# Optimization experiments

Measured on AMD Instinct MI355X. Metric: run time of the kernel, lower is better.

The kernel has to match this reference:

```python
import jax, jax.numpy as jnp
import numpy as np

L = 512          # profile HMM model length (number of match states)
S = 25           # alphabet size (input_dim)
BATCH = 128
T_LEN = 1024
TINY = np.finfo(np.float32).tiny


def setup_inputs():
    key = jax.random.key(0)
    ks = jax.random.split(key, 18)
    def n(k, shape):
        return 0.1 * jax.random.normal(k, shape, dtype=jnp.float32)
    return {
        "seq": jax.random.randint(ks[0], (BATCH, T_LEN), 0, S),
        "em_kernel": n(ks[1], (L, S)),
        "ins_kernel": n(ks[2], (S,)),
        "flank_kernel": n(ks[3], (1,)),
        "btm": n(ks[4], (L,)),
        "m2e": n(ks[5], (L,)),
        "mtm": n(ks[6], (L - 1,)),
        "m2i": n(ks[7], (L - 1,)),
        "i2m": n(ks[8], (L - 1,)),
        "i2i": n(ks[9], (L - 1,)),
        "mtd": n(ks[10], (L,)),
        "dtm": n(ks[11], (L,)),
        "dtd": n(ks[12], (L - 1,)),
        "lf_loop": n(ks[13], (1,)),
        "lf_exit": n(ks[14], (1,)),
        "e2u": n(ks[15], (1,)),
        "e2r": n(ks[16], (1,)),
        "e2t": n(ks[17], (1,)),
    }


def _build_hmm(em_kernel, ins_kernel, flank_kernel, btm, m2e, mtm, m2i, i2m, i2i,
               mtd, dtm, dtd, lf_loop, lf_exit, e2u, e2r, e2t):
    """Build implicit transition matrix A [q,q], emission matrix B [q,S+1], init dist [q].
    Explicit states begin/end/delete are marginalized out (silent states), yielding the
    implicit transition structure of the profile HMM (match skips via delete chains)."""
    Lm = em_kernel.shape[0]
    q = 2 * Lm + 3                      # LF, M_1..M_L, I_1..I_{L-1}, U, RF, T
    U, RF, TM = 2 * Lm, 2 * Lm + 1, 2 * Lm + 2
    idx = jnp.arange(Lm)
    dt = em_kernel.dtype
    # per-source-state softmax over explicit outgoing edges
    begin_p = jax.nn.softmax(jnp.concatenate([btm, mtd[:1]]))            # begin -> M_j / D_1
    btm_p = begin_p[:Lm]
    mp = jax.nn.softmax(jnp.stack([mtm, m2i, m2e[:Lm - 1], mtd[1:]], axis=-1), axis=-1)
    mtm_p, m2i_p, m2e_p, mtd_mid = mp[:, 0], mp[:, 1], mp[:, 2], mp[:, 3]
    ip = jax.nn.softmax(jnp.stack([i2m, i2i], axis=-1), axis=-1)
    i2m_p, i2i_p = ip[:, 0], ip[:, 1]
    dp = jax.nn.softmax(jnp.stack([dtm[:Lm - 1], dtd], axis=-1), axis=-1)
    dtm_p = jnp.concatenate([dp[:, 0], jnp.ones((1,), dt)])              # D_L -> end with prob 1
    dtd_p = dp[:, 1]
    fp = jax.nn.softmax(jnp.concatenate([lf_loop, lf_exit]))            # shared flank kernels
    floop, fexit = fp[0], fp[1]
    ep = jax.nn.softmax(jnp.concatenate([e2u, e2r, e2t]))               # end -> U / RF / T
    # marginalize silent delete chain. Sk[i,k]: P(src_i => target via deletes),
    # src_0 = begin, src_i = M_i; target M_{k+2} for k<=L-2, end for k=L-1.
    mtd_p = jnp.concatenate([begin_p[Lm:], mtd_mid])                    # begin->D_1, M_i->D_{i+1}
    cp_log = jnp.concatenate([jnp.zeros((1,), dt), jnp.cumsum(jnp.log(dtd_p))])
    Sk = mtd_p[:, None] * jnp.exp(cp_log[None, :] - cp_log[:, None]) * dtm_p[None, :]
    Sk = jnp.where(idx[None, :] >= idx[:, None], Sk, jnp.zeros((), dt))
    enter = btm_p + jnp.pad(Sk[0, :Lm - 1], (1, 0))                      # begin => M_j
    begin_end = Sk[0, Lm - 1]                                            # begin => end (all deleted)
    m2e_tot = jnp.concatenate([m2e_p + Sk[1:, Lm - 1], jnp.ones((1,), dt)])
    A = jnp.zeros((q, q), dt)
    Mblk = jnp.zeros((Lm, Lm), dt).at[idx[:-1], idx[1:]].set(mtm_p)
    Mblk = Mblk.at[0:Lm - 1, 1:Lm].add(Sk[1:Lm, 0:Lm - 1])               # match skips (j>=i+2)
    A = A.at[1:Lm + 1, 1:Lm + 1].set(Mblk)
    A = A.at[0, 0].set(floop)
    A = A.at[0, 1:Lm + 1].set(fexit * enter)
    A = A.at[0, U].set(fexit * begin_end * ep[0])
    A = A.at[0, RF].set(fexit * begin_end * ep[1])
    A = A.at[0, TM].set(fexit * begin_end * ep[2])
    A = A.at[jnp.arange(1, Lm), jnp.arange(Lm + 1, 2 * Lm)].set(m2i_p)   # M_i -> I_i
    A = A.at[1:Lm + 1, U].set(m2e_tot * ep[0])
    A = A.at[1:Lm + 1, RF].set(m2e_tot * ep[1])
    A = A.at[1:Lm + 1, TM].set(m2e_tot * ep[2])
    A = A.at[jnp.arange(Lm + 1, 2 * Lm), jnp.arange(2, Lm + 1)].set(i2m_p)  # I_i -> M_{i+1}
    A = A.at[jnp.arange(Lm + 1, 2 * Lm), jnp.arange(Lm + 1, 2 * Lm)].set(i2i_p)
    A = A.at[U, 1:Lm + 1].set(fexit * enter)
    A = A.at[U, U].set(floop + fexit * begin_end * ep[0])
    A = A.at[U, RF].set(fexit * begin_end * ep[1])
    A = A.at[U, TM].set(fexit * begin_end * ep[2])
    A = A.at[RF, RF].set(floop)
    A = A.at[RF, TM].set(fexit)
    A = A.at[TM, TM].set(1.0)
    # emission matrix per make_default_emission_matrix: [ins; em; ins x (L+1)] rows,
    # softmax, zero pad column, terminal one-hot row -> [2L+3, S+1]
    rows = jnp.concatenate([ins_kernel[None], em_kernel,
                            jnp.tile(ins_kernel[None], (Lm + 1, 1))], axis=0)
    Bm = jax.nn.softmax(rows, axis=-1)
    Bm = jnp.concatenate([Bm, jnp.zeros((2 * Lm + 2, 1), dt)], axis=-1)
    s_alph = em_kernel.shape[1]
    Bm = jnp.concatenate([Bm, jax.nn.one_hot(jnp.array([s_alph]), s_alph + 1, dtype=dt)], axis=0)
    # initial distribution: start in left flank w.p. sigmoid(flank_init), else enter model
    p0 = jax.nn.sigmoid(flank_kernel[0])
    init = jnp.zeros((q,), dt).at[0].set(p0)
    init = init.at[1:Lm + 1].set((1 - p0) * enter)
    init = init.at[U].set((1 - p0) * begin_end * ep[0])
    init = init.at[RF].set((1 - p0) * begin_end * ep[1])
    init = init.at[TM].set((1 - p0) * begin_end * ep[2])
    return A, Bm, init


def _forward(seq, *params):
    A, Bm, init = _build_hmm(*params)
    # emission probs per timestep: matvec(B, one_hot(x)) == column gather
    E = Bm.T[seq]                        # [batch, T, q]
    alpha = init[None, :] * E[:, 0]
    s = alpha.sum(-1, keepdims=True) + TINY
    ll = jnp.log(s[:, 0])
    alpha = alpha / s

    def step(carry, Et):
        a, l = carry
        a = Et * (a @ A)                 # forward-algorithm recurrence + scaling
        sn = a.sum(-1, keepdims=True) + TINY
        return (a / sn, l + jnp.log(sn[:, 0])), None

    (alpha, ll), _ = jax.lax.scan(step, (alpha, ll), jnp.swapaxes(E[:, 1:], 0, 1))
    return ll                            # [batch] sequence log-likelihoods


def reference(seq, em_kernel, ins_kernel, flank_kernel, btm, m2e, mtm, m2i, i2m, i2i,
              mtd, dtm, dtd, lf_loop, lf_exit, e2u, e2r, e2t):
    return _forward(seq, em_kernel, ins_kernel, flank_kernel, btm, m2e, mtm, m2i, i2m,
                    i2i, mtd, dtm, dtd, lf_loop, lf_exit, e2u, e2r, e2t)
```

## Files before the change

### kernel.cpp

```cpp
#include <hip/hip_runtime.h>
#include <math.h>

#define LM 512
#define TLEN 1024
#define TINY_F 1.17549435e-38f

#define OFF_ENTER 0
#define OFF_MTM   512
#define OFF_I2M   1024
#define OFF_DTM   1536
#define OFF_WC    2048
#define OFF_MC    2560
#define OFF_M2I   3072
#define OFF_I2I   3584
#define OFF_M2E   4096
#define OFF_INS   4608
#define OFF_SC    4640
#define OFF_EMB   5120

typedef float v2f __attribute__((ext_vector_type(2)));

__device__ __forceinline__ v2f pfma(v2f a, v2f b, v2f c) {
    return __builtin_elementwise_fma(a, b, c);
}
__device__ __forceinline__ v2f vs(float c) { return (v2f){c, c}; }

template<int Ctrl, int RowMask>
__device__ __forceinline__ float fdpp(float oldv, float src) {
    int r = __builtin_amdgcn_update_dpp(
        __builtin_bit_cast(int, oldv), __builtin_bit_cast(int, src),
        Ctrl, RowMask, 0xF, false);
    return __builtin_bit_cast(float, r);
}

template<int Ctrl, int RowMask>
__device__ __forceinline__ float fdppb(float src) {
    int r = __builtin_amdgcn_update_dpp(
        0, __builtin_bit_cast(int, src),
        Ctrl, RowMask, 0xF, true);
    return __builtin_bit_cast(float, r);
}

__device__ __forceinline__ float rdlane63(float v) {
    return __builtin_bit_cast(float,
        __builtin_amdgcn_readlane(__builtin_bit_cast(int, v), 63));
}

__device__ __forceinline__ float wave_sum_to63(float v) {
    v += fdpp<0x111, 0xF>(0.f, v);
    v += fdpp<0x112, 0xF>(0.f, v);
    v += fdpp<0x114, 0xF>(0.f, v);
    v += fdpp<0x118, 0xF>(0.f, v);
    v += fdpp<0x142, 0xA>(0.f, v);
    v += fdpp<0x143, 0xC>(0.f, v);
    return v;
}

__global__ __launch_bounds__(512) void hmm_setup(
    const float* __restrict__ ins,
    const float* __restrict__ flank, const float* __restrict__ btm,
    const float* __restrict__ m2e, const float* __restrict__ mtm,
    const float* __restrict__ m2i, const float* __restrict__ i2m,
    const float* __restrict__ i2i, const float* __restrict__ mtd,
    const float* __restrict__ dtm, const float* __restrict__ dtd,
    const float* __restrict__ lfl, const float* __restrict__ lfe,
    const float* __restrict__ e2u, const float* __restrict__ e2r,
    const float* __restrict__ e2t, float* __restrict__ P)
{
    __shared__ float beginp[513];
    __shared__ float mtdp[512], dtmp[512], dtdp[512], cplog[512];
    __shared__ float mtmp[512], m2ip[512], m2ep[512], i2mp[512], i2ip[512];
    __shared__ float rbuf[512], rbuf2[512];
    const int j = threadIdx.x;

    if (j < 25) {
        float sm = 0.f;
        for (int s = 0; s < 25; ++s) sm += expf(ins[s]);
        P[OFF_INS + j] = log2f(expf(ins[j]) / sm);
    }

    float eb = expf(btm[j]);
    rbuf[j] = eb;
    __syncthreads();
    for (int s = 256; s > 0; s >>= 1) {
        if (j < s) rbuf[j] += rbuf[j + s];
        __syncthreads();
    }
    float e512 = expf(mtd[0]);
    float tot = rbuf[0] + e512;
    beginp[j] = eb / tot;
    if (j == 0) { beginp[512] = e512 / tot; mtdp[0] = e512 / tot; }

    if (j < 511) {
        float a = expf(mtm[j]), b = expf(m2i[j]), c = expf(m2e[j]), d = expf(mtd[j + 1]);
        float s = a + b + c + d;
        mtmp[j] = a / s; m2ip[j] = b / s; m2ep[j] = c / s; mtdp[j + 1] = d / s;
        float ia = expf(i2m[j]), ib = expf(i2i[j]); s = ia + ib;
        i2mp[j] = ia / s; i2ip[j] = ib / s;
        float da = expf(dtm[j]), db = expf(dtd[j]); s = da + db;
        dtmp[j] = da / s; dtdp[j] = db / s;
    }
    if (j == 511) dtmp[511] = 1.0f;
    __syncthreads();

    {
        float lw = (j >= 1) ? logf(dtdp[j - 1]) : 0.f;
        rbuf[j] = lw;
        __syncthreads();
        float* bufs[2] = { rbuf, rbuf2 };
        int cur = 0;
        for (int off = 1; off < 512; off <<= 1) {
            float v = bufs[cur][j];
            if (j >= off) v += bufs[cur][j - off];
            bufs[cur ^ 1][j] = v;
            cur ^= 1;
            __syncthreads();
        }
        cplog[j] = bufs[cur][j];
    }
    __syncthreads();

    if (j == 0) {
        float fl = expf(lfl[0]), fe = expf(lfe[0]); float fs = fl + fe;
        float floop = fl / fs, fexit = fe / fs;
        float eu = expf(e2u[0]), er = expf(e2r[0]), et = expf(e2t[0]);
        float es = eu + er + et; float ep0 = eu / es, ep1 = er / es;
        float p0 = 1.0f / (1.0f + expf(-flank[0]));
        P[OFF_SC + 0] = floop;
        P[OFF_SC + 1] = fexit;
        P[OFF_SC + 2] = p0;
        P[OFF_SC + 5] = ep0;
        P[OFF_SC + 6] = ep1;
        P[OFF_SC + 9] = 1.0f - p0;
    }
    __syncthreads();

    float en = beginp[j];
    if (j >= 1) en += mtdp[0] * expf(cplog[j - 1]) * dtmp[j - 1];
    P[OFF_ENTER + j] = en;
    P[OFF_MTM + j] = (j >= 1) ? mtmp[j - 1] : 0.f;
    P[OFF_I2M + j] = (j >= 1) ? i2mp[j - 1] : 0.f;
    P[OFF_DTM + j] = (j >= 1) ? dtmp[j - 1] : 0.f;
    P[OFF_WC  + j] = (j >= 1) ? mtdp[j]     : 0.f;
    P[OFF_MC  + j] = (j >= 1) ? dtdp[j - 1] : 0.f;
    P[OFF_M2I + j] = (j < 511) ? m2ip[j] : 0.f;
    P[OFF_I2I + j] = (j < 511) ? i2ip[j] : 0.f;
    P[OFF_M2E + j] = (j < 511)
        ? (m2ep[j] + mtdp[j + 1] * expf(cplog[511] - cplog[j + 1]))
        : 1.0f;
}

__global__ __launch_bounds__(64) void hmm_emrel(
    const float* __restrict__ em, const float* __restrict__ ins,
    float* __restrict__ P)
{
    const int j = blockIdx.x * 64 + threadIdx.x;

    float sm = 0.f;
    for (int s = 0; s < 25; ++s) sm += expf(ins[s]);

    const float* row = em + j * 25;
    float mx = row[0];
    for (int s = 1; s < 25; ++s) mx = fmaxf(mx, row[s]);
    float sme = 0.f;
    for (int s = 0; s < 25; ++s) sme += expf(row[s] - mx);
    float inv = 1.0f / sme;

    int lanej = j >> 3, e = j & 7;
    int pos = ((e >> 2) << 8) | (lanej << 2) | (e & 3);
    for (int s = 0; s < 25; ++s) {
        float inspS = expf(ins[s]) / sm;
        P[OFF_EMB + s * 512 + pos] = (expf(row[s] - mx) * inv) / inspS;
    }
}

__global__ __launch_bounds__(64, 1) void hmm_forward(
    const int* __restrict__ seq, const float* __restrict__ P,
    float* __restrict__ out)
{
    __shared__ float sLogEi[32];
    __shared__ __align__(16) int sSeq[TLEN + 4];

    const int lane = threadIdx.x;
    const int b = blockIdx.x;
    const int base = lane * 8;
    const float* __restrict__ EmG = P + OFF_EMB;

    {
        if (lane < 32) sLogEi[lane] = P[OFF_INS + (lane < 25 ? lane : 0)];
        const int4* s4 = (const int4*)(seq + b * TLEN);
        int4* d4 = (int4*)sSeq;
#pragma unroll
        for (int k = lane; k < 256; k += 64) d4[k] = s4[k];
        if (lane < 4) sSeq[TLEN + lane] = 0;
    }
    __syncthreads();

    float llE;
    {
        float le = 0.f;
#pragma unroll
        for (int k = 0; k < 16; ++k) le += sLogEi[sSeq[lane * 16 + k]];
        llE = rdlane63(wave_sum_to63(le));
    }

    float mtm_[8], dtm_[8], wC_[8], mC_[8];
    v2f enter2[4], enterF2[4], m2iS2[4], i2i2[4], m2e2[4], dtmM2[4], invNX2[4];
    {
        float enter_[8], m2iS_[8], i2i_[8], m2e_[8], dtmM_[8], invNX_[8];
#pragma unroll
        for (int e = 0; e < 8; ++e) {
            enter_[e] = P[OFF_ENTER + base + e];
            mtm_[e]   = P[OFF_MTM + base + e];
            dtm_[e]   = P[OFF_DTM + base + e];
            wC_[e]    = P[OFF_WC + base + e];
            mC_[e]    = P[OFF_MC + base + e];
            i2i_[e]   = P[OFF_I2I + base + e];
            m2e_[e]   = P[OFF_M2E + base + e];
            float i2mN = (base + e + 1 < 512) ? P[OFF_I2M + base + e + 1] : 1.0f;
            m2iS_[e]  = P[OFF_M2I + base + e] * i2mN;
            invNX_[e] = 1.0f / i2mN;
        }
        float Mp = mC_[0];
        dtmM_[0] = dtm_[0];
#pragma unroll
        for (int e = 1; e < 8; ++e) { dtmM_[e] = dtm_[e] * Mp; Mp *= mC_[e]; }
#pragma unroll
        for (int p = 0; p < 4; ++p) {
            enter2[p] = (v2f){enter_[2*p], enter_[2*p+1]};
            m2iS2[p]  = (v2f){m2iS_[2*p],  m2iS_[2*p+1]};
            i2i2[p]   = (v2f){i2i_[2*p],   i2i_[2*p+1]};
            m2e2[p]   = (v2f){m2e_[2*p],   m2e_[2*p+1]};
            dtmM2[p]  = (v2f){dtmM_[2*p],  dtmM_[2*p+1]};
            invNX2[p] = (v2f){invNX_[2*p], invNX_[2*p+1]};
        }
    }
    const float floop = P[OFF_SC + 0], fexit = P[OFF_SC + 1], p0 = P[OFF_SC + 2];
    const float ep0 = P[OFF_SC + 5], ep1 = P[OFF_SC + 6];
    const float omp0 = P[OFF_SC + 9];
    const v2f floop2 = vs(floop);
    const v2f epv2 = (v2f){ep0, ep1};
#pragma unroll
    for (int p = 0; p < 4; ++p) enterF2[p] = enter2[p] * vs(fexit);

    v2f am2[4], ci2[4];
#define AM(e) ((e) & 1 ? am2[(e) >> 1].y : am2[(e) >> 1].x)
#define CI(e) ((e) & 1 ? ci2[(e) >> 1].y : ci2[(e) >> 1].x)

    v2f EmA2[4], EmB2[4];
    {
        int s0 = sSeq[0];
        const float4* c4 = (const float4*)(EmG + (s0 << 9) + (lane << 2));
        float4 xx = c4[0], yy = c4[64];
        EmA2[0] = (v2f){xx.x, xx.y}; EmA2[1] = (v2f){xx.z, xx.w};
        EmA2[2] = (v2f){yy.x, yy.y}; EmA2[3] = (v2f){yy.z, yy.w};
    }
#pragma unroll
    for (int p = 0; p < 4; ++p) {
        am2[p] = EmA2[p] * vs(omp0) * enter2[p];
        ci2[p] = (v2f){0.f, 0.f};
    }
    v2f GR = (v2f){p0, 0.f};
    float ll2 = llE;

    int symN = sSeq[1];
    {
        const float4* c4 = (const float4*)(EmG + (symN << 9) + (lane << 2));
        float4 xx = c4[0], yy = c4[64];
        EmA2[0] = (v2f){xx.x, xx.y}; EmA2[1] = (v2f){xx.z, xx.w};
        EmA2[2] = (v2f){yy.x, yy.y}; EmA2[3] = (v2f){yy.z, yy.w};
    }
    symN = sSeq[2];
    int sidx = 3;

#define STEP(EmC2, EmN2, DO_NORM)                                              \
  {                                                                            \
    {    \
      const float4* c4 = (const float4*)(EmG + (symN << 9) + (lane << 2));     \
      float4 xx = c4[0], yy = c4[64];                                          \
      EmN2[0] = (v2f){xx.x, xx.y}; EmN2[1] = (v2f){xx.z, xx.w};                \
      EmN2[2] = (v2f){yy.x, yy.y}; EmN2[3] = (v2f){yy.z, yy.w};                \
      symN = sSeq[sidx]; ++sidx;                                               \
    }                                                                          \
    float amL = fdppb<0x138, 0xF>(am2[3].y);                                   \
    float ciL = fdppb<0x138, 0xF>(ci2[3].y);                                   \
                 \
    float Apre[8];                                                             \
    Apre[0] = amL * wC_[0];                                                    \
    _Pragma("unroll")                                                          \
    for (int e = 1; e < 8; ++e)                                                \
      Apre[e] = fmaf(Apre[e - 1], mC_[e], AM(e - 1) * wC_[e]);                 \
         \
    float carry = fdppb<0x138, 0xF>(Apre[7]);                                  \
                \
    v2f dv = am2[0] * m2e2[0];                                                 \
    dv = pfma(am2[1], m2e2[1], dv);                                            \
    dv = pfma(am2[2], m2e2[2], dv);                                            \
    dv = pfma(am2[3], m2e2[3], dv);                                            \
    float dsum = rdlane63(wave_sum_to63(dv.x + dv.y));                         \
              \
    float Gold = GR.x;                                                         \
    GR = pfma(vs(dsum), epv2, GR * floop2);                                    \
       \
    v2f tp[4];                                                                 \
    tp[0].x = fmaf(amL, mtm_[0], ciL);                                         \
    tp[0].y = fmaf(AM(0), mtm_[1], CI(0));                                     \
    tp[1].x = fmaf(AM(1), mtm_[2], CI(1));                                     \
    tp[1].y = fmaf(AM(2), mtm_[3], CI(2));                                     \
    tp[2].x = fmaf(AM(3), mtm_[4], CI(3));                                     \
    tp[2].y = fmaf(AM(4), mtm_[5], CI(4));                                     \
    tp[3].x = fmaf(AM(5), mtm_[6], CI(5));                                     \
    tp[3].y = fmaf(AM(6), mtm_[7], CI(6));                                     \
                       \
    ci2[0] = pfma(am2[0], m2iS2[0], ci2[0] * i2i2[0]);                         \
    ci2[1] = pfma(am2[1], m2iS2[1], ci2[1] * i2i2[1]);                         \
    ci2[2] = pfma(am2[2], m2iS2[2], ci2[2] * i2i2[2]);                         \
    ci2[3] = pfma(am2[3], m2iS2[3], ci2[3] * i2i2[3]);                         \
          \
    v2f Gold2 = vs(Gold), carry2 = vs(carry);                                  \
    tp[0] = pfma(Gold2, enterF2[0], tp[0]);                                    \
    tp[1] = pfma(Gold2, enterF2[1], tp[1]);                                    \
    tp[2] = pfma(Gold2, enterF2[2], tp[2]);                                    \
    tp[3] = pfma(Gold2, enterF2[3], tp[3]);                                    \
    tp[0].y = fmaf(dtm_[1], Apre[0], tp[0].y);                                 \
    tp[1].x = fmaf(dtm_[2], Apre[1], tp[1].x);                                 \
    tp[1].y = fmaf(dtm_[3], Apre[2], tp[1].y);                                 \
    tp[2].x = fmaf(dtm_[4], Apre[3], tp[2].x);                                 \
    tp[2].y = fmaf(dtm_[5], Apre[4], tp[2].y);                                 \
    tp[3].x = fmaf(dtm_[6], Apre[5], tp[3].x);                                 \
    tp[3].y = fmaf(dtm_[7], Apre[6], tp[3].y);                                 \
    tp[0] = pfma(dtmM2[0], carry2, tp[0]);                                     \
    tp[1] = pfma(dtmM2[1], carry2, tp[1]);                                     \
    tp[2] = pfma(dtmM2[2], carry2, tp[2]);                                     \
    tp[3] = pfma(dtmM2[3], carry2, tp[3]);                                     \
    am2[0] = EmC2[0] * tp[0];                                                  \
    am2[1] = EmC2[1] * tp[1];                                                  \
    am2[2] = EmC2[2] * tp[2];                                                  \
    am2[3] = EmC2[3] * tp[3];                                                  \
      \
                                      \
    if (DO_NORM) {                                                             \
      v2f ns = pfma(ci2[0], invNX2[0], am2[0]);                                \
      ns += pfma(ci2[1], invNX2[1], am2[1]);                                   \
      ns += pfma(ci2[2], invNX2[2], am2[2]);                                   \
      ns += pfma(ci2[3], invNX2[3], am2[3]);                                   \
      float sl = ns.x + ns.y + ((lane == 0) ? (GR.x + GR.y) : 0.f);            \
      float s = rdlane63(wave_sum_to63(sl)) + TINY_F;                          \
      ll2 += __log2f(s);                                                       \
      float inv = 1.0f / s;                                                    \
      v2f inv2 = vs(inv);                                                      \
      am2[0] *= inv2; am2[1] *= inv2; am2[2] *= inv2; am2[3] *= inv2;          \
      ci2[0] *= inv2; ci2[1] *= inv2; ci2[2] *= inv2; ci2[3] *= inv2;          \
      GR *= inv2;                                                              \
    }                                                                          \
  }

#define PAIR(NORM2)                                                            \
    STEP(EmA2, EmB2, 0)                                                        \
    STEP(EmB2, EmA2, NORM2)

    for (int c = 0; c < 63; ++c) {
        int nf = ((c & 3) == 3);
        PAIR(0) PAIR(0) PAIR(0) PAIR(0)
        PAIR(0) PAIR(0) PAIR(0) PAIR(nf)
    }
    for (int p = 0; p < 7; ++p) {
        PAIR(0)
    }
    STEP(EmA2, EmB2, 1)
#undef PAIR
#undef STEP
#undef AM
#undef CI

    if (lane == 0) out[b] = ll2 * 0.69314718055994530942f;
}

extern "C" void kernel_launch(void* const* d_in, const int* in_sizes, int n_in,
                              void* d_out, int out_size, void* d_ws, size_t ws_size,
                              hipStream_t stream) {
    const int*   seq   = (const int*)d_in[0];
    const float* em    = (const float*)d_in[1];
    const float* ins   = (const float*)d_in[2];
    const float* flank = (const float*)d_in[3];
    const float* btm   = (const float*)d_in[4];
    const float* m2e   = (const float*)d_in[5];
    const float* mtm   = (const float*)d_in[6];
    const float* m2i   = (const float*)d_in[7];
    const float* i2m   = (const float*)d_in[8];
    const float* i2i   = (const float*)d_in[9];
    const float* mtd   = (const float*)d_in[10];
    const float* dtm   = (const float*)d_in[11];
    const float* dtd   = (const float*)d_in[12];
    const float* lfl   = (const float*)d_in[13];
    const float* lfe   = (const float*)d_in[14];
    const float* e2u   = (const float*)d_in[15];
    const float* e2r   = (const float*)d_in[16];
    const float* e2t   = (const float*)d_in[17];
    float* P = (float*)d_ws;
    float* out = (float*)d_out;

    hipLaunchKernelGGL(hmm_emrel, dim3(8), dim3(64), 0, stream, em, ins, P);
    hipLaunchKernelGGL(hmm_setup, dim3(1), dim3(512), 0, stream,
        ins, flank, btm, m2e, mtm, m2i, i2m, i2i, mtd, dtm, dtd,
        lfl, lfe, e2u, e2r, e2t, P);
    hipLaunchKernelGGL(hmm_forward, dim3(128), dim3(64), 0, stream, seq, P, out);
}
```

Before: 265.5 us.

## Fuse HMM parameter setup and emission prep into the forward kernel

Replaces the three-launch pipeline (emission prep, parameter setup, forward) with one kernel in which every 64-lane block recomputes the transition parameters in registers, using wave-level DPP scans for the delete-chain prefix sums. The emission table is built directly in LDS (about 51 KB) instead of global workspace, so the per-step emission gathers read LDS rather than global/L2. This removes two kernel launches and the serial dependency between them. In exchange, all 128 blocks redundantly compute the softmaxes and emission table, and register pressure rises during the prologue.

Result: no change. 267.2 us (+0.6%).

```diff
diff --git a/kernel.cpp b/kernel.cpp
--- a/kernel.cpp
+++ b/kernel.cpp
@@ -4,19 +4,6 @@
 #define LM 512
 #define TLEN 1024
 #define TINY_F 1.17549435e-38f
-
-#define OFF_ENTER 0
-#define OFF_MTM   512
-#define OFF_I2M   1024
-#define OFF_DTM   1536
-#define OFF_WC    2048
-#define OFF_MC    2560
-#define OFF_M2I   3072
-#define OFF_I2I   3584
-#define OFF_M2E   4096
-#define OFF_INS   4608
-#define OFF_SC    4640
-#define OFF_EMB   5120
 
 typedef float v2f __attribute__((ext_vector_type(2)));
 
@@ -56,8 +43,9 @@
     return v;
 }
 
-__global__ __launch_bounds__(512) void hmm_setup(
-    const float* __restrict__ ins,
+__global__ __launch_bounds__(64, 1) void hmm_fused(
+    const int* __restrict__ seq,
+    const float* __restrict__ em, const float* __restrict__ ins,
     const float* __restrict__ flank, const float* __restrict__ btm,
     const float* __restrict__ m2e, const float* __restrict__ mtm,
     const float* __restrict__ m2i, const float* __restrict__ i2m,
@@ -65,183 +53,157 @@
     const float* __restrict__ dtm, const float* __restrict__ dtd,
     const float* __restrict__ lfl, const float* __restrict__ lfe,
     const float* __restrict__ e2u, const float* __restrict__ e2r,
-    const float* __restrict__ e2t, float* __restrict__ P)
-{
-    __shared__ float beginp[513];
-    __shared__ float mtdp[512], dtmp[512], dtdp[512], cplog[512];
-    __shared__ float mtmp[512], m2ip[512], m2ep[512], i2mp[512], i2ip[512];
-    __shared__ float rbuf[512], rbuf2[512];
-    const int j = threadIdx.x;
-
-    if (j < 25) {
-        float sm = 0.f;
-        for (int s = 0; s < 25; ++s) sm += expf(ins[s]);
-        P[OFF_INS + j] = log2f(expf(ins[j]) / sm);
-    }
-
-    float eb = expf(btm[j]);
-    rbuf[j] = eb;
-    __syncthreads();
-    for (int s = 256; s > 0; s >>= 1) {
-        if (j < s) rbuf[j] += rbuf[j + s];
-        __syncthreads();
-    }
-    float e512 = expf(mtd[0]);
-    float tot = rbuf[0] + e512;
-    beginp[j] = eb / tot;
-    if (j == 0) { beginp[512] = e512 / tot; mtdp[0] = e512 / tot; }
-
-    if (j < 511) {
-        float a = expf(mtm[j]), b = expf(m2i[j]), c = expf(m2e[j]), d = expf(mtd[j + 1]);
-        float s = a + b + c + d;
-        mtmp[j] = a / s; m2ip[j] = b / s; m2ep[j] = c / s; mtdp[j + 1] = d / s;
-        float ia = expf(i2m[j]), ib = expf(i2i[j]); s = ia + ib;
-        i2mp[j] = ia / s; i2ip[j] = ib / s;
-        float da = expf(dtm[j]), db = expf(dtd[j]); s = da + db;
-        dtmp[j] = da / s; dtdp[j] = db / s;
-    }
-    if (j == 511) dtmp[511] = 1.0f;
-    __syncthreads();
-
-    {
-        float lw = (j >= 1) ? logf(dtdp[j - 1]) : 0.f;
-        rbuf[j] = lw;
-        __syncthreads();
-        float* bufs[2] = { rbuf, rbuf2 };
-        int cur = 0;
-        for (int off = 1; off < 512; off <<= 1) {
-            float v = bufs[cur][j];
-            if (j >= off) v += bufs[cur][j - off];
-            bufs[cur ^ 1][j] = v;
-            cur ^= 1;
-            __syncthreads();
-        }
-        cplog[j] = bufs[cur][j];
-    }
-    __syncthreads();
-
-    if (j == 0) {
-        float fl = expf(lfl[0]), fe = expf(lfe[0]); float fs = fl + fe;
-        float floop = fl / fs, fexit = fe / fs;
-        float eu = expf(e2u[0]), er = expf(e2r[0]), et = expf(e2t[0]);
-        float es = eu + er + et; float ep0 = eu / es, ep1 = er / es;
-        float p0 = 1.0f / (1.0f + expf(-flank[0]));
-        P[OFF_SC + 0] = floop;
-        P[OFF_SC + 1] = fexit;
-        P[OFF_SC + 2] = p0;
-        P[OFF_SC + 5] = ep0;
-        P[OFF_SC + 6] = ep1;
-        P[OFF_SC + 9] = 1.0f - p0;
-    }
-    __syncthreads();
-
-    float en = beginp[j];
-    if (j >= 1) en += mtdp[0] * expf(cplog[j - 1]) * dtmp[j - 1];
-    P[OFF_ENTER + j] = en;
-    P[OFF_MTM + j] = (j >= 1) ? mtmp[j - 1] : 0.f;
-    P[OFF_I2M + j] = (j >= 1) ? i2mp[j - 1] : 0.f;
-    P[OFF_DTM + j] = (j >= 1) ? dtmp[j - 1] : 0.f;
-    P[OFF_WC  + j] = (j >= 1) ? mtdp[j]     : 0.f;
-    P[OFF_MC  + j] = (j >= 1) ? dtdp[j - 1] : 0.f;
-    P[OFF_M2I + j] = (j < 511) ? m2ip[j] : 0.f;
-    P[OFF_I2I + j] = (j < 511) ? i2ip[j] : 0.f;
-    P[OFF_M2E + j] = (j < 511)
-        ? (m2ep[j] + mtdp[j + 1] * expf(cplog[511] - cplog[j + 1]))
-        : 1.0f;
-}
-
-__global__ __launch_bounds__(64) void hmm_emrel(
-    const float* __restrict__ em, const float* __restrict__ ins,
-    float* __restrict__ P)
-{
-    const int j = blockIdx.x * 64 + threadIdx.x;
-
-    float sm = 0.f;
-    for (int s = 0; s < 25; ++s) sm += expf(ins[s]);
-
-    const float* row = em + j * 25;
-    float mx = row[0];
-    for (int s = 1; s < 25; ++s) mx = fmaxf(mx, row[s]);
-    float sme = 0.f;
-    for (int s = 0; s < 25; ++s) sme += expf(row[s] - mx);
-    float inv = 1.0f / sme;
-
-    int lanej = j >> 3, e = j & 7;
-    int pos = ((e >> 2) << 8) | (lanej << 2) | (e & 3);
-    for (int s = 0; s < 25; ++s) {
-        float inspS = expf(ins[s]) / sm;
-        P[OFF_EMB + s * 512 + pos] = (expf(row[s] - mx) * inv) / inspS;
-    }
-}
-
-__global__ __launch_bounds__(64, 1) void hmm_forward(
-    const int* __restrict__ seq, const float* __restrict__ P,
+    const float* __restrict__ e2t,
     float* __restrict__ out)
 {
+    __shared__ __align__(16) float sEmb[25 * 512];
     __shared__ float sLogEi[32];
     __shared__ __align__(16) int sSeq[TLEN + 4];
 
     const int lane = threadIdx.x;
     const int b = blockIdx.x;
     const int base = lane * 8;
-    const float* __restrict__ EmG = P + OFF_EMB;
-
-    {
-        if (lane < 32) sLogEi[lane] = P[OFF_INS + (lane < 25 ? lane : 0)];
+
+    {
         const int4* s4 = (const int4*)(seq + b * TLEN);
         int4* d4 = (int4*)sSeq;
 #pragma unroll
         for (int k = lane; k < 256; k += 64) d4[k] = s4[k];
         if (lane < 4) sSeq[TLEN + lane] = 0;
     }
-    __syncthreads();
-
-    float llE;
-    {
-        float le = 0.f;
-#pragma unroll
-        for (int k = 0; k < 16; ++k) le += sLogEi[sSeq[lane * 16 + k]];
-        llE = rdlane63(wave_sum_to63(le));
-    }
-
-    float mtm_[8], dtm_[8], wC_[8], mC_[8];
-    v2f enter2[4], enterF2[4], m2iS2[4], i2i2[4], m2e2[4], dtmM2[4], invNX2[4];
-    {
-        float enter_[8], m2iS_[8], i2i_[8], m2e_[8], dtmM_[8], invNX_[8];
+
+    float insp[25];
+    {
+        float smI = 0.f;
+#pragma unroll
+        for (int s = 0; s < 25; ++s) smI += expf(ins[s]);
+#pragma unroll
+        for (int s = 0; s < 25; ++s) insp[s] = expf(ins[s]) / smI;
+        if (lane < 25) sLogEi[lane] = log2f(insp[lane]);
+    }
+
+    const float flv = expf(lfl[0]), fev = expf(lfe[0]);
+    const float fsv = flv + fev;
+    const float floop = flv / fsv, fexit = fev / fsv;
+    const float eu = expf(e2u[0]), er = expf(e2r[0]), et = expf(e2t[0]);
+    const float esv = eu + er + et;
+    const float ep0 = eu / esv, ep1 = er / esv;
+    const float p0 = 1.0f / (1.0f + expf(-flank[0]));
+    const float omp0 = 1.0f - p0;
+
+    float mtm_[8], dtm_[8], wC_[8], mC_[8], dtmM_[8];
+    float i2iA[8], m2iSA[8], invNXA[8], m2eA[8], enterA[8];
+    {
+        float lw[8], plocal[8], ebv[8], m2epJ[8], mtdpJ1[8], lwn[8];
 #pragma unroll
         for (int e = 0; e < 8; ++e) {
-            enter_[e] = P[OFF_ENTER + base + e];
-            mtm_[e]   = P[OFF_MTM + base + e];
-            dtm_[e]   = P[OFF_DTM + base + e];
-            wC_[e]    = P[OFF_WC + base + e];
-            mC_[e]    = P[OFF_MC + base + e];
-            i2i_[e]   = P[OFF_I2I + base + e];
-            m2e_[e]   = P[OFF_M2E + base + e];
-            float i2mN = (base + e + 1 < 512) ? P[OFF_I2M + base + e + 1] : 1.0f;
-            m2iS_[e]  = P[OFF_M2I + base + e] * i2mN;
-            invNX_[e] = 1.0f / i2mN;
+            const int j = base + e;
+            const int jm1 = (j >= 1) ? j - 1 : 0;
+            const int jc  = (j < 511) ? j : 510;
+            {
+                float a = expf(mtm[jm1]), bb = expf(m2i[jm1]);
+                float c = expf(m2e[jm1]), d = expf(mtd[jm1 + 1]);
+                float s4 = a + bb + c + d;
+                mtm_[e] = (j >= 1) ? a / s4 : 0.f;
+                wC_[e]  = (j >= 1) ? d / s4 : 0.f;
+                float da = expf(dtm[jm1]), db = expf(dtd[jm1]);
+                float sd = da + db;
+                float dtv = da / sd, mcv = db / sd;
+                dtm_[e] = (j >= 1) ? dtv : 0.f;
+                mC_[e]  = (j >= 1) ? mcv : 0.f;
+                lw[e]   = (j >= 1) ? logf(mcv) : 0.f;
+            }
+            {
+                float a = expf(mtm[jc]), bb = expf(m2i[jc]);
+                float c = expf(m2e[jc]), d = expf(mtd[jc + 1]);
+                float s4 = a + bb + c + d;
+                float m2ip = bb / s4;
+                m2epJ[e]  = c / s4;
+                mtdpJ1[e] = d / s4;
+                float ia = expf(i2m[jc]), ib = expf(i2i[jc]);
+                float s2 = ia + ib;
+                float i2mp = ia / s2;
+                i2iA[e] = (j < 511) ? ib / s2 : 0.f;
+                float da = expf(dtm[jc]), db = expf(dtd[jc]);
+                float sd = da + db;
+                lwn[e] = logf(db / sd);
+                float i2mN = (j + 1 < 512) ? i2mp : 1.0f;
+                m2iSA[e]  = ((j < 511) ? m2ip : 0.f) * i2mN;
+                invNXA[e] = 1.0f / i2mN;
+            }
+            ebv[e] = expf(btm[j]);
+            plocal[e] = (e == 0) ? lw[0] : plocal[e - 1] + lw[e];
+        }
+        float incl = wave_sum_to63(plocal[7]);
+        float excl = fdppb<0x138, 0xF>(incl);
+        float cpT  = rdlane63(incl);
+        float ebl = ebv[0] + ebv[1] + ebv[2] + ebv[3]
+                  + ebv[4] + ebv[5] + ebv[6] + ebv[7];
+        float e512 = expf(mtd[0]);
+        float tot = rdlane63(wave_sum_to63(ebl)) + e512;
+        float mtdp0 = e512 / tot;
+#pragma unroll
+        for (int e = 0; e < 8; ++e) {
+            const int j = base + e;
+            float beginp = ebv[e] / tot;
+            float cpjm1 = (e == 0) ? excl : excl + plocal[e - 1];
+            enterA[e] = beginp
+                + ((j >= 1) ? mtdp0 * expf(cpjm1) * dtm_[e] : 0.f);
+            float cpj = excl + plocal[e];
+            m2eA[e] = (j < 511)
+                ? (m2epJ[e] + mtdpJ1[e] * expf(cpT - (cpj + lwn[e])))
+                : 1.0f;
         }
         float Mp = mC_[0];
         dtmM_[0] = dtm_[0];
 #pragma unroll
         for (int e = 1; e < 8; ++e) { dtmM_[e] = dtm_[e] * Mp; Mp *= mC_[e]; }
-#pragma unroll
-        for (int p = 0; p < 4; ++p) {
-            enter2[p] = (v2f){enter_[2*p], enter_[2*p+1]};
-            m2iS2[p]  = (v2f){m2iS_[2*p],  m2iS_[2*p+1]};
-            i2i2[p]   = (v2f){i2i_[2*p],   i2i_[2*p+1]};
-            m2e2[p]   = (v2f){m2e_[2*p],   m2e_[2*p+1]};
-            dtmM2[p]  = (v2f){dtmM_[2*p],  dtmM_[2*p+1]};
-            invNX2[p] = (v2f){invNX_[2*p], invNX_[2*p+1]};
+    }
+
+    {
+#pragma unroll
+        for (int e = 0; e < 8; ++e) {
+            const int j = base + e;
+            const float* row = em + j * 25;
+            float r[25], ex[25];
+#pragma unroll
+            for (int s = 0; s < 25; ++s) r[s] = row[s];
+            float mx = r[0];
+#pragma unroll
+            for (int s = 1; s < 25; ++s) mx = fmaxf(mx, r[s]);
+            float sme = 0.f;
+#pragma unroll
+            for (int s = 0; s < 25; ++s) { ex[s] = expf(r[s] - mx); sme += ex[s]; }
+            float inv = 1.0f / sme;
+            const int pos = ((e >> 2) << 8) | (lane << 2) | (e & 3);
+#pragma unroll
+            for (int s = 0; s < 25; ++s)
+                sEmb[s * 512 + pos] = (ex[s] * inv) / insp[s];
         }
     }
-    const float floop = P[OFF_SC + 0], fexit = P[OFF_SC + 1], p0 = P[OFF_SC + 2];
-    const float ep0 = P[OFF_SC + 5], ep1 = P[OFF_SC + 6];
-    const float omp0 = P[OFF_SC + 9];
+    __syncthreads();
+
+    float llE;
+    {
+        float le = 0.f;
+#pragma unroll
+        for (int k = 0; k < 16; ++k) le += sLogEi[sSeq[lane * 16 + k]];
+        llE = rdlane63(wave_sum_to63(le));
+    }
+
+    v2f enter2[4], enterF2[4], m2iS2[4], i2i2[4], m2e2[4], dtmM2[4], invNX2[4];
+#pragma unroll
+    for (int p = 0; p < 4; ++p) {
+        enter2[p]  = (v2f){enterA[2*p], enterA[2*p+1]};
+        enterF2[p] = enter2[p] * vs(fexit);
+        m2iS2[p]   = (v2f){m2iSA[2*p], m2iSA[2*p+1]};
+        i2i2[p]    = (v2f){i2iA[2*p],  i2iA[2*p+1]};
+        m2e2[p]    = (v2f){m2eA[2*p],  m2eA[2*p+1]};
+        dtmM2[p]   = (v2f){dtmM_[2*p], dtmM_[2*p+1]};
+        invNX2[p]  = (v2f){invNXA[2*p], invNXA[2*p+1]};
+    }
     const v2f floop2 = vs(floop);
     const v2f epv2 = (v2f){ep0, ep1};
-#pragma unroll
-    for (int p = 0; p < 4; ++p) enterF2[p] = enter2[p] * vs(fexit);
 
     v2f am2[4], ci2[4];
 #define AM(e) ((e) & 1 ? am2[(e) >> 1].y : am2[(e) >> 1].x)
@@ -250,7 +212,7 @@
     v2f EmA2[4], EmB2[4];
     {
         int s0 = sSeq[0];
-        const float4* c4 = (const float4*)(EmG + (s0 << 9) + (lane << 2));
+        const float4* c4 = (const float4*)(sEmb + (s0 << 9) + (lane << 2));
         float4 xx = c4[0], yy = c4[64];
         EmA2[0] = (v2f){xx.x, xx.y}; EmA2[1] = (v2f){xx.z, xx.w};
         EmA2[2] = (v2f){yy.x, yy.y}; EmA2[3] = (v2f){yy.z, yy.w};
@@ -265,7 +227,7 @@
 
     int symN = sSeq[1];
     {
-        const float4* c4 = (const float4*)(EmG + (symN << 9) + (lane << 2));
+        const float4* c4 = (const float4*)(sEmb + (symN << 9) + (lane << 2));
         float4 xx = c4[0], yy = c4[64];
         EmA2[0] = (v2f){xx.x, xx.y}; EmA2[1] = (v2f){xx.z, xx.w};
         EmA2[2] = (v2f){yy.x, yy.y}; EmA2[3] = (v2f){yy.z, yy.w};
@@ -275,8 +237,8 @@
 
 #define STEP(EmC2, EmN2, DO_NORM)                                              \
   {                                                                            \
-    {    \
-      const float4* c4 = (const float4*)(EmG + (symN << 9) + (lane << 2));     \
+    {                \
+      const float4* c4 = (const float4*)(sEmb + (symN << 9) + (lane << 2));    \
       float4 xx = c4[0], yy = c4[64];                                          \
       EmN2[0] = (v2f){xx.x, xx.y}; EmN2[1] = (v2f){xx.z, xx.w};                \
       EmN2[2] = (v2f){yy.x, yy.y}; EmN2[3] = (v2f){yy.z, yy.w};                \
@@ -337,8 +299,7 @@
     am2[1] = EmC2[1] * tp[1];                                                  \
     am2[2] = EmC2[2] * tp[2];                                                  \
     am2[3] = EmC2[3] * tp[3];                                                  \
-      \
-                                      \
+              \
     if (DO_NORM) {                                                             \
       v2f ns = pfma(ci2[0], invNX2[0], am2[0]);                                \
       ns += pfma(ci2[1], invNX2[1], am2[1]);                                   \
@@ -397,12 +358,10 @@
     const float* e2u   = (const float*)d_in[15];
     const float* e2r   = (const float*)d_in[16];
     const float* e2t   = (const float*)d_in[17];
-    float* P = (float*)d_ws;
     float* out = (float*)d_out;
-
-    hipLaunchKernelGGL(hmm_emrel, dim3(8), dim3(64), 0, stream, em, ins, P);
-    hipLaunchKernelGGL(hmm_setup, dim3(1), dim3(512), 0, stream,
-        ins, flank, btm, m2e, mtm, m2i, i2m, i2i, mtd, dtm, dtd,
-        lfl, lfe, e2u, e2r, e2t, P);
-    hipLaunchKernelGGL(hmm_forward, dim3(128), dim3(64), 0, stream, seq, P, out);
-}
+    (void)d_ws; (void)ws_size;
+
+    hipLaunchKernelGGL(hmm_fused, dim3(128), dim3(64), 0, stream,
+        seq, em, ins, flank, btm, m2e, mtm, m2i, i2m, i2i, mtd, dtm, dtd,
+        lfl, lfe, e2u, e2r, e2t, out);
+}
```
